# Kernel optimization log

Hardware: AMD Instinct MI355X
Metric: run time of the kernel (lower is better)

The kernel has to match this reference:

```python
import jax, jax.numpy as jnp
import numpy as np

N, Wt, Tt, DIM = 16, 256, 2048, 256
EPS = 1e-5

def silu(x):
    return x * jax.nn.sigmoid(x)

def setup_inputs() -> dict:
    key = jax.random.key(0)
    ks = jax.random.split(key, 12)
    d = {}
    d['T'] = jnp.arange(Tt, dtype=jnp.float32)
    d['durations'] = jax.random.uniform(ks[0], (N, Wt, 1), jnp.float32)
    d['features'] = jax.random.normal(ks[1], (N, Wt, DIM), jnp.float32)
    d['conv1_w'] = jax.random.normal(ks[2], (8, DIM, 3), jnp.float32) * 0.05
    d['conv1_b'] = jnp.zeros((8,), jnp.float32)
    d['bn1_g'] = jnp.ones((8,), jnp.float32)
    d['bn1_b'] = jnp.zeros((8,), jnp.float32)
    d['bn1_m'] = jnp.zeros((8,), jnp.float32)
    d['bn1_v'] = jnp.ones((8,), jnp.float32)
    d['conv2_w'] = jax.random.normal(ks[3], (8, DIM, 3), jnp.float32) * 0.05
    d['conv2_b'] = jnp.zeros((8,), jnp.float32)
    d['bn2_g'] = jnp.ones((8,), jnp.float32)
    d['bn2_b'] = jnp.zeros((8,), jnp.float32)
    d['bn2_m'] = jnp.zeros((8,), jnp.float32)
    d['bn2_v'] = jnp.ones((8,), jnp.float32)
    d['sb1_w1'] = jax.random.normal(ks[4], (10, 2), jnp.float32) * 0.3
    d['sb1_b1'] = jnp.zeros((2,), jnp.float32)
    d['sb1_w2'] = jax.random.normal(ks[5], (2, 2), jnp.float32) * 0.3
    d['sb1_b2'] = jnp.zeros((2,), jnp.float32)
    d['sb2_w1'] = jax.random.normal(ks[6], (10, 16), jnp.float32) * 0.3
    d['sb2_b1'] = jnp.zeros((16,), jnp.float32)
    d['sb2_w2'] = jax.random.normal(ks[7], (16, 16), jnp.float32) * 0.3
    d['sb2_b2'] = jnp.zeros((16,), jnp.float32)
    d['proj1_w'] = jax.random.normal(ks[8], (2, DIM), jnp.float32) * 0.3
    d['proj1_b'] = jnp.zeros((DIM,), jnp.float32)
    d['proj2_w'] = jax.random.normal(ks[9], (16, 1), jnp.float32) * 0.3
    d['proj2_b'] = jnp.zeros((1,), jnp.float32)
    return d

def _conv_bn_silu(x_ncw, w, b, g, beta, m, v):
    # Conv1d(dim->8, k=3, pad=1) + BatchNorm(eval) + SiLU
    y = jax.lax.conv_general_dilated(x_ncw, w, (1,), [(1, 1)],
                                     dimension_numbers=('NCH', 'OIH', 'NCH'))
    y = y + b[None, :, None]
    y = (y - m[None, :, None]) * jax.lax.rsqrt(v[None, :, None] + EPS)
    y = y * g[None, :, None] + beta[None, :, None]
    return silu(y)

def _swish_block(x, w1, b1, w2, b2):
    x = silu(x @ w1 + b1)
    return silu(x @ w2 + b2)

def reference(T, durations, features, conv1_w, conv1_b, bn1_g, bn1_b, bn1_m, bn1_v,
              conv2_w, conv2_b, bn2_g, bn2_b, bn2_m, bn2_v,
              sb1_w1, sb1_b1, sb1_w2, sb1_b2, sb2_w1, sb2_b1, sb2_w2, sb2_b2,
              proj1_w, proj1_b, proj2_w, proj2_b):
    feat = jnp.swapaxes(features, 1, 2)  # (N, C, W)
    n, _, w = feat.shape
    t = T.shape[0]
    left = jnp.swapaxes(_conv_bn_silu(feat, conv1_w, conv1_b, bn1_g, bn1_b, bn1_m, bn1_v), 1, 2)   # (N, W, 8)
    right = jnp.swapaxes(_conv_bn_silu(feat, conv2_w, conv2_b, bn2_g, bn2_b, bn2_m, bn2_v), 1, 2)  # (N, W, 8)
    token_end = jnp.cumsum(durations, axis=1)        # (N, W, 1)
    token_start = token_end - durations              # (N, W, 1)
    S = T[None, None, :] - token_start               # (N, W, T)
    E = token_end - T[None, None, :]                 # (N, W, T)
    left_b = jnp.broadcast_to(left[:, :, None, :], (n, w, t, 8))
    right_b = jnp.broadcast_to(right[:, :, None, :], (n, w, t, 8))
    xleft = jnp.concatenate([S[..., None], E[..., None], left_b], axis=-1)    # (N, W, T, 10)
    xright = jnp.concatenate([S[..., None], E[..., None], right_b], axis=-1)  # (N, W, T, 10)
    C = _swish_block(xleft, sb1_w1, sb1_b1, sb1_w2, sb1_b2)                   # (N, W, T, 2)
    xr = _swish_block(xright, sb2_w1, sb2_b1, sb2_w2, sb2_b2)                 # (N, W, T, 16)
    score = (xr @ proj2_w + proj2_b)[..., 0]                                  # (N, W, T)
    Wsm = jax.nn.softmax(score, axis=1)  # softmax over tokens W
    out_r = jnp.einsum('nkt,ndk->ntd', Wsm, feat)                             # (N, T, dim)
    out_l = jnp.einsum('nkt,nktp->ntp', Wsm, C) @ proj1_w + proj1_b           # (N, T, dim)
    return out_l + out_r
```

## Files before the change

### kernel.cpp

```cpp
#include <hip/hip_runtime.h>
#include <hip/hip_bf16.h>

#define NN  16
#define WT  256
#define TT  2048
#define DIM 256
#define TBT 8
#define TB2 32

__device__ __forceinline__ float fast_rcp(float x){ return __builtin_amdgcn_rcpf(x); }

__device__ __forceinline__ float silu_f(float x){
    return x * fast_rcp(1.0f + __expf(-x));
}

__device__ __forceinline__ void fma4(float4& a, float s, const float4& f){
    a.x = fmaf(s, f.x, a.x); a.y = fmaf(s, f.y, a.y);
    a.z = fmaf(s, f.z, a.z); a.w = fmaf(s, f.w, a.w);
}

__global__ __launch_bounds__(WT) void cumsum_k(const float* __restrict__ dur,
                                               float* __restrict__ ts,
                                               float* __restrict__ te){
    int n = blockIdx.x, w = threadIdx.x;
    __shared__ float s[WT];
    float d = dur[n*WT + w];
    s[w] = d;
    __syncthreads();
    for (int off = 1; off < WT; off <<= 1){
        float v = (w >= off) ? s[w-off] : 0.0f;
        __syncthreads();
        s[w] += v;
        __syncthreads();
    }
    float e = s[w];
    te[n*WT + w] = e;
    ts[n*WT + w] = e - d;
}

__global__ __launch_bounds__(256) void prep_k(
    const float* __restrict__ feat,
    const float* __restrict__ c1w, const float* __restrict__ c1b,
    const float* __restrict__ g1,  const float* __restrict__ be1,
    const float* __restrict__ m1,  const float* __restrict__ vv1,
    const float* __restrict__ c2w, const float* __restrict__ c2b,
    const float* __restrict__ g2,  const float* __restrict__ be2,
    const float* __restrict__ m2,  const float* __restrict__ vv2,
    const float* __restrict__ sb1w1, const float* __restrict__ sb1b1,
    const float* __restrict__ sb2w1, const float* __restrict__ sb2b1,
    const float* __restrict__ ts, const float* __restrict__ te,
    float* __restrict__ v1o, float* __restrict__ v2o)
{
    int w = blockIdx.x, n = blockIdx.y;
    int tid = threadIdx.x;
    const float* fb = feat + (size_t)(n*WT)*DIM;
    float fm = (w > 0)    ? fb[(size_t)(w-1)*DIM + tid] : 0.0f;
    float f0 =              fb[(size_t) w   *DIM + tid];
    float fp = (w < WT-1) ? fb[(size_t)(w+1)*DIM + tid] : 0.0f;

    float pl[8], pr[8];
    #pragma unroll
    for (int o = 0; o < 8; o++){
        const float* wp = c1w + (size_t)(o*DIM + tid)*3;
        pl[o] = fmaf(fm, wp[0], fmaf(f0, wp[1], fp*wp[2]));
        const float* wq = c2w + (size_t)(o*DIM + tid)*3;
        pr[o] = fmaf(fm, wq[0], fmaf(f0, wq[1], fp*wq[2]));
    }
    #pragma unroll
    for (int o = 0; o < 8; o++){
        #pragma unroll
        for (int off = 32; off; off >>= 1){
            pl[o] += __shfl_xor(pl[o], off);
            pr[o] += __shfl_xor(pr[o], off);
        }
    }
    __shared__ float sws[4][16];
    int wave = tid >> 6, lane = tid & 63;
    if (lane == 0){
        #pragma unroll
        for (int o = 0; o < 8; o++){ sws[wave][o] = pl[o]; sws[wave][8+o] = pr[o]; }
    }
    __syncthreads();
    __shared__ float slr[16];
    if (tid < 16){
        float s = sws[0][tid] + sws[1][tid] + sws[2][tid] + sws[3][tid];
        int o = tid & 7; bool isr = tid >= 8;
        float bias = isr ? c2b[o] : c1b[o];
        float mm   = isr ? m2[o]  : m1[o];
        float vv   = isr ? vv2[o] : vv1[o];
        float gg   = isr ? g2[o]  : g1[o];
        float bb   = isr ? be2[o] : be1[o];
        float y = s + bias;
        y = (y - mm) * rsqrtf(vv + 1e-5f);
        y = y * gg + bb;
        slr[tid] = silu_f(y);
    }
    __syncthreads();
    float start = ts[n*WT + w], end = te[n*WT + w];
    if (tid < 16){
        int j = tid;
        float acc = sb2b1[j] - start*sb2w1[j] + end*sb2w1[16 + j];
        #pragma unroll
        for (int o = 0; o < 8; o++) acc = fmaf(slr[8+o], sb2w1[(2+o)*16 + j], acc);
        v2o[(size_t)(n*WT + w)*16 + j] = acc;
    } else if (tid < 18){
        int p = tid - 16;
        float acc = sb1b1[p] - start*sb1w1[p] + end*sb1w1[2 + p];
        #pragma unroll
        for (int o = 0; o < 8; o++) acc = fmaf(slr[o], sb1w1[(2+o)*2 + p], acc);
        v1o[(size_t)(n*WT + w)*2 + p] = acc;
    }
}

__global__ __launch_bounds__(256) void score_k(
    const float* __restrict__ Tg,
    const float* __restrict__ v1g, const float* __restrict__ v2g,
    const float* __restrict__ sb1w1, const float* __restrict__ sb1w2, const float* __restrict__ sb1b2,
    const float* __restrict__ sb2w1, const float* __restrict__ sb2w2, const float* __restrict__ sb2b2,
    const float* __restrict__ p2w, const float* __restrict__ p2b,
    float* __restrict__ wsm_g, float* __restrict__ wc_g)
{
    int n   = blockIdx.y;
    int t0  = blockIdx.x * TBT;
    int tid = threadIdx.x;
    int w   = tid;
    int lane = tid & 63, wave = tid >> 6;

    __shared__ float s_w2[16*16];
    __shared__ float s_u2[16], s_b2[16], s_p2w[16];
    __shared__ float s_u1[2], s_w21[4], s_b21[2];
    __shared__ float s_xa[4][TBT];
    __shared__ float s_xs[4][TBT];
    __shared__ float s_xc0[4][TBT], s_xc1[4][TBT];

    s_w2[tid] = sb2w2[tid];
    if (tid < 16){
        s_u2[tid]  = sb2w1[tid] - sb2w1[16 + tid];
        s_b2[tid]  = sb2b2[tid];
        s_p2w[tid] = p2w[tid];
    } else if (tid < 18){
        int p = tid - 16;
        s_u1[p]  = sb1w1[p] - sb1w1[2 + p];
        s_b21[p] = sb1b2[p];
    } else if (tid < 22){
        s_w21[tid - 18] = sb1w2[tid - 18];
    }
    __syncthreads();

    float v2r[16];
    {
        const float4* vp = (const float4*)(v2g + (size_t)(n*WT + w)*16);
        float4 a = vp[0], b = vp[1], c = vp[2], d = vp[3];
        v2r[0]=a.x; v2r[1]=a.y; v2r[2]=a.z; v2r[3]=a.w;
        v2r[4]=b.x; v2r[5]=b.y; v2r[6]=b.z; v2r[7]=b.w;
        v2r[8]=c.x; v2r[9]=c.y; v2r[10]=c.z; v2r[11]=c.w;
        v2r[12]=d.x; v2r[13]=d.y; v2r[14]=d.z; v2r[15]=d.w;
    }
    float v1r0, v1r1;
    {
        const float* vp = v1g + (size_t)(n*WT + w)*2;
        v1r0 = vp[0]; v1r1 = vp[1];
    }
    float p2bv = p2b[0];
    float tv[TBT];
    #pragma unroll
    for (int ti = 0; ti < TBT; ti++) tv[ti] = Tg[t0 + ti];

    float scores[TBT];
    #pragma unroll
    for (int tp = 0; tp < TBT; tp += 2){
        float h2a[16], h2b[16];
        #pragma unroll
        for (int j = 0; j < 16; j++){ float b = s_b2[j]; h2a[j] = b; h2b[j] = b; }
        #pragma unroll
        for (int i = 0; i < 16; i++){
            float u = s_u2[i], v = v2r[i];
            float aa = silu_f(fmaf(tv[tp],   u, v));
            float ab = silu_f(fmaf(tv[tp+1], u, v));
            #pragma unroll
            for (int j = 0; j < 16; j++){
                float wv = s_w2[i*16 + j];
                h2a[j] = fmaf(aa, wv, h2a[j]);
                h2b[j] = fmaf(ab, wv, h2b[j]);
            }
        }
        float sa = p2bv, sb = p2bv;
        #pragma unroll
        for (int j = 0; j < 16; j++){
            float pw = s_p2w[j];
            sa = fmaf(silu_f(h2a[j]), pw, sa);
            sb = fmaf(silu_f(h2b[j]), pw, sb);
        }
        scores[tp] = sa; scores[tp+1] = sb;
    }

    float c0r[TBT], c1r[TBT];
    {
        float u10 = s_u1[0], u11 = s_u1[1];
        float w00 = s_w21[0], w01 = s_w21[1], w10 = s_w21[2], w11 = s_w21[3];
        float b0 = s_b21[0], b1 = s_b21[1];
        #pragma unroll
        for (int ti = 0; ti < TBT; ti++){
            float gl0 = silu_f(fmaf(tv[ti], u10, v1r0));
            float gl1 = silu_f(fmaf(tv[ti], u11, v1r1));
            c0r[ti] = silu_f(fmaf(gl0, w00, fmaf(gl1, w10, b0)));
            c1r[ti] = silu_f(fmaf(gl0, w01, fmaf(gl1, w11, b1)));
        }
    }

    float m[TBT];
    #pragma unroll
    for (int ti = 0; ti < TBT; ti++) m[ti] = scores[ti];
    #pragma unroll
    for (int off = 32; off; off >>= 1){
        #pragma unroll
        for (int ti = 0; ti < TBT; ti++) m[ti] = fmaxf(m[ti], __shfl_xor(m[ti], off));
    }
    if (lane == 0){
        #pragma unroll
        for (int ti = 0; ti < TBT; ti++) s_xa[wave][ti] = m[ti];
    }
    __syncthreads();
    #pragma unroll
    for (int ti = 0; ti < TBT; ti++)
        m[ti] = fmaxf(fmaxf(s_xa[0][ti], s_xa[1][ti]), fmaxf(s_xa[2][ti], s_xa[3][ti]));

    float e[TBT], ps[TBT], pc0[TBT], pc1[TBT];
    #pragma unroll
    for (int ti = 0; ti < TBT; ti++){
        e[ti]   = __expf(scores[ti] - m[ti]);
        ps[ti]  = e[ti];
        pc0[ti] = e[ti] * c0r[ti];
        pc1[ti] = e[ti] * c1r[ti];
    }
    #pragma unroll
    for (int off = 32; off; off >>= 1){
        #pragma unroll
        for (int ti = 0; ti < TBT; ti++){
            ps[ti]  += __shfl_xor(ps[ti],  off);
            pc0[ti] += __shfl_xor(pc0[ti], off);
            pc1[ti] += __shfl_xor(pc1[ti], off);
        }
    }
    if (lane == 0){
        #pragma unroll
        for (int ti = 0; ti < TBT; ti++){
            s_xs[wave][ti]  = ps[ti];
            s_xc0[wave][ti] = pc0[ti];
            s_xc1[wave][ti] = pc1[ti];
        }
    }
    __syncthreads();

    float* wbase = wsm_g + ((size_t)n*TT + t0)*WT + w;
    #pragma unroll
    for (int ti = 0; ti < TBT; ti++){
        float S  = s_xs[0][ti] + s_xs[1][ti] + s_xs[2][ti] + s_xs[3][ti];
        float rS = fast_rcp(S);
        wbase[(size_t)ti*WT] = e[ti] * rS;
    }
    if (tid < TBT){
        int ti = tid;
        float S  = s_xs[0][ti] + s_xs[1][ti] + s_xs[2][ti] + s_xs[3][ti];
        float rS = fast_rcp(S);
        float2 wc;
        wc.x = (s_xc0[0][ti] + s_xc0[1][ti] + s_xc0[2][ti] + s_xc0[3][ti]) * rS;
        wc.y = (s_xc1[0][ti] + s_xc1[1][ti] + s_xc1[2][ti] + s_xc1[3][ti]) * rS;
        *(float2*)(wc_g + ((size_t)n*TT + t0 + ti)*2) = wc;
    }
}

__global__ __launch_bounds__(256) void outr_k(
    const float* __restrict__ feat, const float* __restrict__ wsm_g,
    const float* __restrict__ wc_g,
    const float* __restrict__ p1w, const float* __restrict__ p1b,
    float* __restrict__ out)
{
    int n   = blockIdx.y;
    int t0  = blockIdx.x * TB2;
    int tid = threadIdx.x;
    int lane = tid & 63, wv = tid >> 6;
    int dq  = lane * 4;

    __shared__ float s_wsm[TB2][WT];

    const float4* wbase = (const float4*)(wsm_g + ((size_t)n*TT + t0)*WT);
    #pragma unroll
    for (int i = tid; i < TB2*WT/4; i += 256){
        int idx = i * 4;
        *(float4*)&s_wsm[idx >> 8][idx & 255] = wbase[i];
    }
    __syncthreads();

    const float* fbase = feat + (size_t)n*WT*DIM + dq;
    int tb = wv * 8;
    float4 acc[8];
    #pragma unroll
    for (int k = 0; k < 8; k++) acc[k] = make_float4(0.f, 0.f, 0.f, 0.f);

    #pragma unroll 4
    for (int w0 = 0; w0 < WT; w0++){
        float4 f = *(const float4*)(fbase + (size_t)w0*DIM);
        #pragma unroll
        for (int k = 0; k < 8; k++)
            fma4(acc[k], s_wsm[tb + k][w0], f);
    }

    float4 pw0 = *(const float4*)(p1w + dq);
    float4 pw1 = *(const float4*)(p1w + DIM + dq);
    float4 pb  = *(const float4*)(p1b + dq);
    float* obase = out + ((size_t)n*TT + t0 + tb)*DIM + dq;
    const float* wcb = wc_g + ((size_t)n*TT + t0 + tb)*2;
    #pragma unroll
    for (int k = 0; k < 8; k++){
        float wc0 = wcb[2*k], wc1 = wcb[2*k + 1];
        float4 r;
        r.x = fmaf(wc0, pw0.x, fmaf(wc1, pw1.x, acc[k].x + pb.x));
        r.y = fmaf(wc0, pw0.y, fmaf(wc1, pw1.y, acc[k].y + pb.y));
        r.z = fmaf(wc0, pw0.z, fmaf(wc1, pw1.z, acc[k].z + pb.z));
        r.w = fmaf(wc0, pw0.w, fmaf(wc1, pw1.w, acc[k].w + pb.w));
        *(float4*)(obase + (size_t)k*DIM) = r;
    }
}

__global__ __launch_bounds__(256) void fused_k(
    const float* __restrict__ Tg, const float* __restrict__ feat,
    const float* __restrict__ v1g, const float* __restrict__ v2g,
    const float* __restrict__ sb1w1, const float* __restrict__ sb1w2, const float* __restrict__ sb1b2,
    const float* __restrict__ sb2w1, const float* __restrict__ sb2w2, const float* __restrict__ sb2b2,
    const float* __restrict__ p1w, const float* __restrict__ p1b,
    const float* __restrict__ p2w, const float* __restrict__ p2b,
    float* __restrict__ out)
{
    int n   = blockIdx.y;
    int t0  = blockIdx.x * TBT;
    int tid = threadIdx.x;
    int w   = tid;
    int lane = tid & 63, wave = tid >> 6;

    __shared__ float s_w2[16*16];
    __shared__ float s_u2[16], s_b2[16], s_p2w[16];
    __shared__ float s_u1[2], s_w21[4], s_b21[2];
    __shared__ float s_wsmT[WT][TBT];
    __shared__ float s_xa[4][TBT];
    __shared__ float s_xs[4][TBT];
    __shared__ float s_xc0[4][TBT], s_xc1[4][TBT];
    __shared__ float s_wc0[TBT], s_wc1[TBT];
    __shared__ float s_out[4][DIM];

    s_w2[tid] = sb2w2[tid];
    if (tid < 16){
        s_u2[tid]  = sb2w1[tid] - sb2w1[16 + tid];
        s_b2[tid]  = sb2b2[tid];
        s_p2w[tid] = p2w[tid];
    } else if (tid < 18){
        int p = tid - 16;
        s_u1[p]  = sb1w1[p] - sb1w1[2 + p];
        s_b21[p] = sb1b2[p];
    } else if (tid < 22){
        s_w21[tid - 18] = sb1w2[tid - 18];
    }
    __syncthreads();

    float v2r[16];
    {
        const float4* vp = (const float4*)(v2g + (size_t)(n*WT + w)*16);
        float4 a = vp[0], b = vp[1], c = vp[2], d = vp[3];
        v2r[0]=a.x; v2r[1]=a.y; v2r[2]=a.z; v2r[3]=a.w;
        v2r[4]=b.x; v2r[5]=b.y; v2r[6]=b.z; v2r[7]=b.w;
        v2r[8]=c.x; v2r[9]=c.y; v2r[10]=c.z; v2r[11]=c.w;
        v2r[12]=d.x; v2r[13]=d.y; v2r[14]=d.z; v2r[15]=d.w;
    }
    float v1r0, v1r1;
    {
        const float* vp = v1g + (size_t)(n*WT + w)*2;
        v1r0 = vp[0]; v1r1 = vp[1];
    }
    float p2bv = p2b[0];
    float tv[TBT];
    #pragma unroll
    for (int ti = 0; ti < TBT; ti++) tv[ti] = Tg[t0 + ti];

    float scores[TBT];
    #pragma unroll
    for (int tp = 0; tp < TBT; tp += 2){
        float h2a[16], h2b[16];
        #pragma unroll
        for (int j = 0; j < 16; j++){ float b = s_b2[j]; h2a[j] = b; h2b[j] = b; }
        #pragma unroll
        for (int i = 0; i < 16; i++){
            float u = s_u2[i], v = v2r[i];
            float aa = silu_f(fmaf(tv[tp],   u, v));
            float ab = silu_f(fmaf(tv[tp+1], u, v));
            #pragma unroll
            for (int j = 0; j < 16; j++){
                float wv = s_w2[i*16 + j];
                h2a[j] = fmaf(aa, wv, h2a[j]);
                h2b[j] = fmaf(ab, wv, h2b[j]);
            }
        }
        float sa = p2bv, sb = p2bv;
        #pragma unroll
        for (int j = 0; j < 16; j++){
            float pw = s_p2w[j];
            sa = fmaf(silu_f(h2a[j]), pw, sa);
            sb = fmaf(silu_f(h2b[j]), pw, sb);
        }
        scores[tp] = sa; scores[tp+1] = sb;
    }

    float c0r[TBT], c1r[TBT];
    {
        float u10 = s_u1[0], u11 = s_u1[1];
        float w00 = s_w21[0], w01 = s_w21[1], w10 = s_w21[2], w11 = s_w21[3];
        float b0 = s_b21[0], b1 = s_b21[1];
        #pragma unroll
        for (int ti = 0; ti < TBT; ti++){
            float gl0 = silu_f(fmaf(tv[ti], u10, v1r0));
            float gl1 = silu_f(fmaf(tv[ti], u11, v1r1));
            c0r[ti] = silu_f(fmaf(gl0, w00, fmaf(gl1, w10, b0)));
            c1r[ti] = silu_f(fmaf(gl0, w01, fmaf(gl1, w11, b1)));
        }
    }

    float m[TBT];
    #pragma unroll
    for (int ti = 0; ti < TBT; ti++) m[ti] = scores[ti];
    #pragma unroll
    for (int off = 32; off; off >>= 1){
        #pragma unroll
        for (int ti = 0; ti < TBT; ti++) m[ti] = fmaxf(m[ti], __shfl_xor(m[ti], off));
    }
    if (lane == 0){
        #pragma unroll
        for (int ti = 0; ti < TBT; ti++) s_xa[wave][ti] = m[ti];
    }
    __syncthreads();
    #pragma unroll
    for (int ti = 0; ti < TBT; ti++)
        m[ti] = fmaxf(fmaxf(s_xa[0][ti], s_xa[1][ti]), fmaxf(s_xa[2][ti], s_xa[3][ti]));

    float e[TBT], ps[TBT], pc0[TBT], pc1[TBT];
    #pragma unroll
    for (int ti = 0; ti < TBT; ti++){
        e[ti]  = __expf(scores[ti] - m[ti]);
        ps[ti] = e[ti];
        pc0[ti] = e[ti] * c0r[ti];
        pc1[ti] = e[ti] * c1r[ti];
    }
    #pragma unroll
    for (int off = 32; off; off >>= 1){
        #pragma unroll
        for (int ti = 0; ti < TBT; ti++){
            ps[ti]  += __shfl_xor(ps[ti],  off);
            pc0[ti] += __shfl_xor(pc0[ti], off);
            pc1[ti] += __shfl_xor(pc1[ti], off);
        }
    }
    if (lane == 0){
        #pragma unroll
        for (int ti = 0; ti < TBT; ti++){
            s_xs[wave][ti]  = ps[ti];
            s_xc0[wave][ti] = pc0[ti];
            s_xc1[wave][ti] = pc1[ti];
        }
    }
    __syncthreads();
    #pragma unroll
    for (int ti = 0; ti < TBT; ti++){
        float S  = s_xs[0][ti] + s_xs[1][ti] + s_xs[2][ti] + s_xs[3][ti];
        float rS = fast_rcp(S);
        s_wsmT[w][ti] = e[ti] * rS;
    }
    if (tid < TBT){
        int ti = tid;
        float S  = s_xs[0][ti] + s_xs[1][ti] + s_xs[2][ti] + s_xs[3][ti];
        float rS = fast_rcp(S);
        s_wc0[ti] = (s_xc0[0][ti] + s_xc0[1][ti] + s_xc0[2][ti] + s_xc0[3][ti]) * rS;
        s_wc1[ti] = (s_xc1[0][ti] + s_xc1[1][ti] + s_xc1[2][ti] + s_xc1[3][ti]) * rS;
    }
    __syncthreads();

    int wid = wave;
    int dq  = lane;
    const float* fbase = feat + (size_t)n*WT*DIM + dq*4;
    float4 acc[TBT];
    #pragma unroll
    for (int i = 0; i < TBT; i++) acc[i] = make_float4(0.f, 0.f, 0.f, 0.f);

    #pragma unroll 4
    for (int w0 = wid; w0 < WT; w0 += 4){
        float4 f = *(const float4*)(fbase + (size_t)w0*DIM);
        const float4* wp = (const float4*)&s_wsmT[w0][0];
        float4 wA = wp[0], wB = wp[1];
        fma4(acc[0], wA.x, f); fma4(acc[1], wA.y, f);
        fma4(acc[2], wA.z, f); fma4(acc[3], wA.w, f);
        fma4(acc[4], wB.x, f); fma4(acc[5], wB.y, f);
        fma4(acc[6], wB.z, f); fma4(acc[7], wB.w, f);
    }

    float pw0 = p1w[tid], pw1 = p1w[DIM + tid], pbv = p1b[tid];
    float* orow = out + ((size_t)n*TT + t0)*DIM;
    #pragma unroll
    for (int ti = 0; ti < TBT; ti++){
        __syncthreads();
        *(float4*)&s_out[wid][dq*4] = acc[ti];
        __syncthreads();
        float r = s_out[0][tid] + s_out[1][tid] + s_out[2][tid] + s_out[3][tid];
        float o = fmaf(s_wc0[ti], pw0, fmaf(s_wc1[ti], pw1, r + pbv));
        orow[(size_t)ti*DIM + tid] = o;
    }
}

extern "C" void kernel_launch(void* const* d_in, const int* in_sizes, int n_in,
                              void* d_out, int out_size, void* d_ws, size_t ws_size,
                              hipStream_t stream)
{
    const float* Tg    = (const float*)d_in[0];
    const float* dur   = (const float*)d_in[1];
    const float* feat  = (const float*)d_in[2];
    const float* c1w   = (const float*)d_in[3];
    const float* c1b   = (const float*)d_in[4];
    const float* bn1g  = (const float*)d_in[5];
    const float* bn1b  = (const float*)d_in[6];
    const float* bn1m  = (const float*)d_in[7];
    const float* bn1v  = (const float*)d_in[8];
    const float* c2w   = (const float*)d_in[9];
    const float* c2b   = (const float*)d_in[10];
    const float* bn2g  = (const float*)d_in[11];
    const float* bn2b  = (const float*)d_in[12];
    const float* bn2m  = (const float*)d_in[13];
    const float* bn2v  = (const float*)d_in[14];
    const float* sb1w1 = (const float*)d_in[15];
    const float* sb1b1 = (const float*)d_in[16];
    const float* sb1w2 = (const float*)d_in[17];
    const float* sb1b2 = (const float*)d_in[18];
    const float* sb2w1 = (const float*)d_in[19];
    const float* sb2b1 = (const float*)d_in[20];
    const float* sb2w2 = (const float*)d_in[21];
    const float* sb2b2 = (const float*)d_in[22];
    const float* p1w   = (const float*)d_in[23];
    const float* p1b   = (const float*)d_in[24];
    const float* p2w   = (const float*)d_in[25];
    const float* p2b   = (const float*)d_in[26];
    float* out = (float*)d_out;

    float* ws = (float*)d_ws;
    float* ts  = ws;
    float* te  = ws + 4096;
    float* v1  = ws + 8192;
    float* v2  = ws + 16384;
    float* wc  = ws + 16384 + 65536;
    float* wsm = ws + 16384 + 65536 + 65536;
    size_t need = ((size_t)16384 + 65536 + 65536 + (size_t)NN*TT*WT) * sizeof(float);

    cumsum_k<<<NN, WT, 0, stream>>>(dur, ts, te);
    prep_k<<<dim3(WT, NN), 256, 0, stream>>>(feat, c1w, c1b, bn1g, bn1b, bn1m, bn1v,
                                             c2w, c2b, bn2g, bn2b, bn2m, bn2v,
                                             sb1w1, sb1b1, sb2w1, sb2b1, ts, te, v1, v2);
    if (ws_size >= need){
        score_k<<<dim3(TT/TBT, NN), 256, 0, stream>>>(Tg, v1, v2,
                                                      sb1w1, sb1w2, sb1b2,
                                                      sb2w1, sb2w2, sb2b2,
                                                      p2w, p2b, wsm, wc);
        outr_k<<<dim3(TT/TB2, NN), 256, 0, stream>>>(feat, wsm, wc, p1w, p1b, out);
    } else {
        fused_k<<<dim3(TT/TBT, NN), 256, 0, stream>>>(Tg, feat, v1, v2,
                                                      sb1w1, sb1w2, sb1b2,
                                                      sb2w1, sb2w2, sb2b2,
                                                      p1w, p1b, p2w, p2b, out);
    }
}
```

Measured before the change: 319.6 us.

## Compute feature-weighted output with bf16 MFMA and pack features into bf16 tiles

Replaces the scalar FP32 outr_k kernel with an MFMA 16x16x32 bf16 kernel. The softmax weights are now stored as bf16, which halves their global write and read traffic. A new featpack_k kernel converts the features to bf16 in a K-blocked layout suited to MFMA operand loads. The cost is lower precision in the weights and features, plus one extra small kernel launch.

```diff
diff --git a/kernel.cpp b/kernel.cpp
--- a/kernel.cpp
+++ b/kernel.cpp
@@ -6,12 +6,20 @@
 #define TT  2048
 #define DIM 256
 #define TBT 8
-#define TB2 32
+
+typedef __attribute__((ext_vector_type(8))) short short8_t;
+typedef __attribute__((ext_vector_type(4))) float f32x4;
 
 __device__ __forceinline__ float fast_rcp(float x){ return __builtin_amdgcn_rcpf(x); }
 
 __device__ __forceinline__ float silu_f(float x){
     return x * fast_rcp(1.0f + __expf(-x));
+}
+
+__device__ __forceinline__ unsigned short f2bf(float x){
+    union { float f; unsigned u; } v; v.f = x;
+    unsigned r = v.u + 0x7FFFu + ((v.u >> 16) & 1u);
+    return (unsigned short)(r >> 16);
 }
 
 __device__ __forceinline__ void fma4(float4& a, float s, const float4& f){
@@ -112,13 +120,34 @@
     }
 }
 
+__global__ __launch_bounds__(256) void featpack_k(const float* __restrict__ feat,
+                                                  unsigned short* __restrict__ featP)
+{
+    int kb = blockIdx.x, n = blockIdx.y;
+    int d = threadIdx.x;
+    const float* fb = feat + (size_t)n*WT*DIM + (size_t)kb*32*DIM + d;
+    unsigned short* op = featP + ((size_t)(n*8 + kb)*DIM + d)*32;
+    unsigned short buf[32];
+    #pragma unroll
+    for (int e = 0; e < 32; e++) buf[e] = f2bf(fb[(size_t)e*DIM]);
+    #pragma unroll
+    for (int g = 0; g < 4; g++){
+        uint4 u;
+        u.x = (unsigned)buf[g*8+0] | ((unsigned)buf[g*8+1] << 16);
+        u.y = (unsigned)buf[g*8+2] | ((unsigned)buf[g*8+3] << 16);
+        u.z = (unsigned)buf[g*8+4] | ((unsigned)buf[g*8+5] << 16);
+        u.w = (unsigned)buf[g*8+6] | ((unsigned)buf[g*8+7] << 16);
+        *(uint4*)(op + g*8) = u;
+    }
+}
+
 __global__ __launch_bounds__(256) void score_k(
     const float* __restrict__ Tg,
     const float* __restrict__ v1g, const float* __restrict__ v2g,
     const float* __restrict__ sb1w1, const float* __restrict__ sb1w2, const float* __restrict__ sb1b2,
     const float* __restrict__ sb2w1, const float* __restrict__ sb2w2, const float* __restrict__ sb2b2,
     const float* __restrict__ p2w, const float* __restrict__ p2b,
-    float* __restrict__ wsm_g, float* __restrict__ wc_g)
+    unsigned short* __restrict__ wsm_b, float* __restrict__ wc_g)
 {
     int n   = blockIdx.y;
     int t0  = blockIdx.x * TBT;
@@ -252,12 +281,12 @@
     }
     __syncthreads();
 
-    float* wbase = wsm_g + ((size_t)n*TT + t0)*WT + w;
+    unsigned short* wbase = wsm_b + ((size_t)n*TT + t0)*WT + w;
     #pragma unroll
     for (int ti = 0; ti < TBT; ti++){
         float S  = s_xs[0][ti] + s_xs[1][ti] + s_xs[2][ti] + s_xs[3][ti];
         float rS = fast_rcp(S);
-        wbase[(size_t)ti*WT] = e[ti] * rS;
+        wbase[(size_t)ti*WT] = f2bf(e[ti] * rS);
     }
     if (tid < TBT){
         int ti = tid;
@@ -270,56 +299,52 @@
     }
 }
 
-__global__ __launch_bounds__(256) void outr_k(
-    const float* __restrict__ feat, const float* __restrict__ wsm_g,
+__global__ __launch_bounds__(256) void outr_mfma_k(
+    const unsigned short* __restrict__ wsmB, const unsigned short* __restrict__ featP,
     const float* __restrict__ wc_g,
     const float* __restrict__ p1w, const float* __restrict__ p1b,
     float* __restrict__ out)
 {
-    int n   = blockIdx.y;
-    int t0  = blockIdx.x * TB2;
-    int tid = threadIdx.x;
-    int lane = tid & 63, wv = tid >> 6;
-    int dq  = lane * 4;
-
-    __shared__ float s_wsm[TB2][WT];
-
-    const float4* wbase = (const float4*)(wsm_g + ((size_t)n*TT + t0)*WT);
-    #pragma unroll
-    for (int i = tid; i < TB2*WT/4; i += 256){
-        int idx = i * 4;
-        *(float4*)&s_wsm[idx >> 8][idx & 255] = wbase[i];
-    }
-    __syncthreads();
-
-    const float* fbase = feat + (size_t)n*WT*DIM + dq;
-    int tb = wv * 8;
-    float4 acc[8];
-    #pragma unroll
-    for (int k = 0; k < 8; k++) acc[k] = make_float4(0.f, 0.f, 0.f, 0.f);
-
-    #pragma unroll 4
-    for (int w0 = 0; w0 < WT; w0++){
-        float4 f = *(const float4*)(fbase + (size_t)w0*DIM);
-        #pragma unroll
-        for (int k = 0; k < 8; k++)
-            fma4(acc[k], s_wsm[tb + k][w0], f);
-    }
-
-    float4 pw0 = *(const float4*)(p1w + dq);
-    float4 pw1 = *(const float4*)(p1w + DIM + dq);
-    float4 pb  = *(const float4*)(p1b + dq);
-    float* obase = out + ((size_t)n*TT + t0 + tb)*DIM + dq;
-    const float* wcb = wc_g + ((size_t)n*TT + t0 + tb)*2;
-    #pragma unroll
-    for (int k = 0; k < 8; k++){
-        float wc0 = wcb[2*k], wc1 = wcb[2*k + 1];
-        float4 r;
-        r.x = fmaf(wc0, pw0.x, fmaf(wc1, pw1.x, acc[k].x + pb.x));
-        r.y = fmaf(wc0, pw0.y, fmaf(wc1, pw1.y, acc[k].y + pb.y));
-        r.z = fmaf(wc0, pw0.z, fmaf(wc1, pw1.z, acc[k].z + pb.z));
-        r.w = fmaf(wc0, pw0.w, fmaf(wc1, pw1.w, acc[k].w + pb.w));
-        *(float4*)(obase + (size_t)k*DIM) = r;
+    int n    = blockIdx.y;
+    int t0   = blockIdx.x * 64;
+    int tid  = threadIdx.x;
+    int lane = tid & 63, wave = tid >> 6;
+    int tw   = t0 + wave*16;
+    int l15  = lane & 15, quad = lane >> 4;
+
+    f32x4 acc[16];
+    #pragma unroll
+    for (int dt = 0; dt < 16; dt++) acc[dt] = (f32x4){0.f, 0.f, 0.f, 0.f};
+
+    const unsigned short* aPtr = wsmB + ((size_t)(n*TT + tw + l15))*WT + quad*8;
+
+    #pragma unroll
+    for (int kb = 0; kb < 8; kb++){
+        short8_t af = *(const short8_t*)(aPtr + kb*32);
+        const unsigned short* bp = featP + ((size_t)(n*8 + kb)*DIM + l15)*32 + quad*8;
+        #pragma unroll
+        for (int dt = 0; dt < 16; dt++){
+            short8_t bf = *(const short8_t*)(bp + (size_t)dt*16*32);
+            acc[dt] = __builtin_amdgcn_mfma_f32_16x16x32_bf16(af, bf, acc[dt], 0, 0, 0);
+        }
+    }
+
+    float wc0[4], wc1[4];
+    #pragma unroll
+    for (int r = 0; r < 4; r++){
+        const float* wp = wc_g + ((size_t)(n*TT + tw + quad*4 + r))*2;
+        wc0[r] = wp[0]; wc1[r] = wp[1];
+    }
+    float* obase = out + ((size_t)(n*TT + tw + quad*4))*DIM;
+    #pragma unroll
+    for (int dt = 0; dt < 16; dt++){
+        int d = dt*16 + l15;
+        float pa = p1w[d], pb2 = p1w[DIM + d], pc = p1b[d];
+        #pragma unroll
+        for (int r = 0; r < 4; r++){
+            float val = acc[dt][r] + fmaf(wc0[r], pa, fmaf(wc1[r], pb2, pc));
+            obase[(size_t)r*DIM + d] = val;
+        }
     }
 }
 
@@ -551,19 +576,22 @@
     float* v1  = ws + 8192;
     float* v2  = ws + 16384;
     float* wc  = ws + 16384 + 65536;
-    float* wsm = ws + 16384 + 65536 + 65536;
-    size_t need = ((size_t)16384 + 65536 + 65536 + (size_t)NN*TT*WT) * sizeof(float);
+    unsigned short* wsmB  = (unsigned short*)(ws + 16384 + 65536 + 65536);
+    unsigned short* featP = wsmB + (size_t)NN*TT*WT;
+    size_t need = ((size_t)16384 + 65536 + 65536)*sizeof(float)
+                + ((size_t)NN*TT*WT + (size_t)NN*WT*DIM)*sizeof(unsigned short);
 
     cumsum_k<<<NN, WT, 0, stream>>>(dur, ts, te);
     prep_k<<<dim3(WT, NN), 256, 0, stream>>>(feat, c1w, c1b, bn1g, bn1b, bn1m, bn1v,
                                              c2w, c2b, bn2g, bn2b, bn2m, bn2v,
                                              sb1w1, sb1b1, sb2w1, sb2b1, ts, te, v1, v2);
     if (ws_size >= need){
+        featpack_k<<<dim3(8, NN), 256, 0, stream>>>(feat, featP);
         score_k<<<dim3(TT/TBT, NN), 256, 0, stream>>>(Tg, v1, v2,
                                                       sb1w1, sb1w2, sb1b2,
                                                       sb2w1, sb2w2, sb2b2,
-                                                      p2w, p2b, wsm, wc);
-        outr_k<<<dim3(TT/TB2, NN), 256, 0, stream>>>(feat, wsm, wc, p1w, p1b, out);
+                                                      p2w, p2b, wsmB, wc);
+        outr_mfma_k<<<dim3(TT/64, NN), 256, 0, stream>>>(wsmB, featP, wc, p1w, p1b, out);
     } else {
         fused_k<<<dim3(TT/TBT, NN), 256, 0, stream>>>(Tg, feat, v1, v2,
                                                       sb1w1, sb1w2, sb1b2,
```

Result: faster. 310.4 us (-2.9%).
